# Kernel tuning notes

Measured on AMD Instinct MI355X. Metric: run time of the kernel, lower is better.

Reference implementation:

```python
import jax, jax.numpy as jnp
import numpy as np

B, W, C, N = 2, 2048, 512, 8
K = C // N                      # 64
HALF = K * (K + 1) // 2 - K     # strict upper-triangle count
EPS = 1e-5


def _layernorm(x, gamma, beta):
    mu = jnp.mean(x, axis=-1, keepdims=True)
    var = jnp.mean(jnp.square(x - mu), axis=-1, keepdims=True)
    return (x - mu) * jax.lax.rsqrt(var + EPS) * gamma + beta


def _build_metric(halves, diagonals):
    # symmetric per-head metric: strict upper triangle from `halves`,
    # mirrored, diagonal overwritten by `diagonals` (diag of m+m^T is 0).
    iu0, iu1 = np.triu_indices(K, k=1)
    m = jnp.zeros((N, K, K), dtype=halves.dtype).at[:, iu0, iu1].set(halves)
    m = m + jnp.swapaxes(m, -1, -2)
    d = np.arange(K)
    return m.at[:, d, d].set(diagonals)


def setup_inputs() -> dict:
    key = jax.random.key(0)
    ks = jax.random.split(key, 9)
    return {
        "x1": jax.random.normal(ks[0], (B, W, C), jnp.float32),
        "x2": jax.random.normal(ks[1], (B, W, C), jnp.float32),
        "gamma": jnp.ones((C,), jnp.float32),
        "beta": jnp.zeros((C,), jnp.float32),
        "proj_nck": jax.random.normal(ks[2], (N, C, K), jnp.float32) * (C ** -0.5),
        "halves": jax.random.normal(ks[3], (N, HALF), jnp.float32) * 0.05,
        "diagonals": jax.random.normal(ks[4], (N, K), jnp.float32) * 0.05,
        "W_mixer": jax.random.normal(ks[5], (C, C), jnp.float32) * 0.02,
        "b_mixer": jnp.zeros((C,), jnp.float32),
    }


def reference(x1, x2, gamma, beta, proj_nck, halves, diagonals, W_mixer, b_mixer):
    x1n = _layernorm(x1, gamma, beta)
    x2n = _layernorm(x2, gamma, beta)
    metric_nkk = _build_metric(halves, diagonals)

    # per-head projections (same projection used for both sequences)
    p1_bnwk = jnp.einsum("bwc,nck->bnwk", x1n, proj_nck)
    p2_bnwk = jnp.einsum("bwc,nck->bnwk", x2n, proj_nck)

    # bilinear metric scores  Q . M . K^T  -> [B, N, W, W]
    dots_bnww = jnp.einsum("bnwk,nkj,bnvj->bnwv", p1_bnwk, metric_nkk, p2_bnwk)

    # NOTE: the original computes a scaled/masked softmax of dots_bnww but
    # never uses it for the output; the value mix uses the RAW dot products.
    # We omit the dead softmax — output math is identical.

    nudged_bnwk = jnp.einsum("bnwv,bnvk->bnwk", dots_bnww, p1_bnwk)
    nudged_bwc = jnp.transpose(nudged_bnwk, (0, 2, 1, 3)).reshape(x1.shape[0], x1.shape[1], C)
    return nudged_bwc @ W_mixer.T + b_mixer
```

## Files before the change

kernel.cpp:

```cpp
#include <hip/hip_runtime.h>

typedef unsigned short u16;
typedef __attribute__((ext_vector_type(8))) short short8;
typedef __attribute__((ext_vector_type(4))) float f32x4;

#define HALFN 2016

__device__ __forceinline__ u16 f2b_rn(float x) {
    union { float f; unsigned u; } v; v.f = x;
    unsigned r = v.u + 0x7FFFu + ((v.u >> 16) & 1u);
    return (u16)(r >> 16);
}

__device__ __forceinline__ void gll16(const void* g, void* s) {
    __builtin_amdgcn_global_load_lds(
        (const __attribute__((address_space(1))) unsigned int*)g,
        (__attribute__((address_space(3))) unsigned int*)s, 16, 0, 0);
}

__global__ __launch_bounds__(256) void ln_prep(const float* __restrict__ x1,
                                               const float* __restrict__ x2,
                                               const float* __restrict__ gamma,
                                               const float* __restrict__ beta,
                                               const float* __restrict__ proj,
                                               u16* __restrict__ Xh,
                                               u16* __restrict__ Pwh,
                                               float* __restrict__ S) {
    const int bid = blockIdx.x, t = threadIdx.x;

    if (bid < 2048) {
        const int wv = t >> 6, lane = t & 63;
        const int row = bid * 4 + wv;
        const float* src = (row < 4096) ? (x1 + (size_t)row * 512)
                                        : (x2 + (size_t)(row - 4096) * 512);
        float4 v0 = *(const float4*)&src[lane * 4];
        float4 v1 = *(const float4*)&src[256 + lane * 4];
        float s  = v0.x + v0.y + v0.z + v0.w + v1.x + v1.y + v1.z + v1.w;
        float sq = v0.x * v0.x + v0.y * v0.y + v0.z * v0.z + v0.w * v0.w +
                   v1.x * v1.x + v1.y * v1.y + v1.z * v1.z + v1.w * v1.w;
        #pragma unroll
        for (int off = 32; off > 0; off >>= 1) {
            s  += __shfl_down(s, off);
            sq += __shfl_down(sq, off);
        }
        s  = __shfl(s, 0);
        sq = __shfl(sq, 0);
        float mu  = s * (1.0f / 512.0f);
        float var = sq * (1.0f / 512.0f) - mu * mu;
        float rs  = rsqrtf(var + 1e-5f);
        float4 g0 = *(const float4*)&gamma[lane * 4];
        float4 g1 = *(const float4*)&gamma[256 + lane * 4];
        float4 b0 = *(const float4*)&beta[lane * 4];
        float4 b1 = *(const float4*)&beta[256 + lane * 4];
        ushort4 h0, h1;
        h0.x = f2b_rn((v0.x - mu) * rs * g0.x + b0.x);
        h0.y = f2b_rn((v0.y - mu) * rs * g0.y + b0.y);
        h0.z = f2b_rn((v0.z - mu) * rs * g0.z + b0.z);
        h0.w = f2b_rn((v0.w - mu) * rs * g0.w + b0.w);
        h1.x = f2b_rn((v1.x - mu) * rs * g1.x + b1.x);
        h1.y = f2b_rn((v1.y - mu) * rs * g1.y + b1.y);
        h1.z = f2b_rn((v1.z - mu) * rs * g1.z + b1.z);
        h1.w = f2b_rn((v1.w - mu) * rs * g1.w + b1.w);
        *(ushort4*)&Xh[(size_t)row * 512 + lane * 4] = h0;
        *(ushort4*)&Xh[(size_t)row * 512 + 256 + lane * 4] = h1;
    } else if (bid < 2112) {
        __shared__ float tile[64][65];
        const int id = bid - 2048;
        const int n = id >> 3, c0 = (id & 7) * 64;
        #pragma unroll
        for (int i = 0; i < 4; i++) {
            int flat = i * 256 + t;
            int c = flat >> 4, k4 = (flat & 15) * 4;
            float4 v = *(const float4*)&proj[(size_t)n * 32768 + (size_t)(c0 + c) * 64 + k4];
            tile[c][k4 + 0] = v.x; tile[c][k4 + 1] = v.y;
            tile[c][k4 + 2] = v.z; tile[c][k4 + 3] = v.w;
        }
        __syncthreads();
        #pragma unroll
        for (int i = 0; i < 16; i++) {
            int flat = i * 256 + t;
            int k = flat >> 6, c = flat & 63;
            Pwh[(size_t)(n * 64 + k) * 512 + c0 + c] = f2b_rn(tile[c][k]);
        }
    } else {
        float4 z = {0.f, 0.f, 0.f, 0.f};
        #pragma unroll
        for (int i = 0; i < 64; i++)
            *(float4*)&S[(size_t)(i * 256 + t) * 4] = z;
    }
}

template<int TM, int TN>
__device__ __forceinline__ void gemm_core_bk64(const u16* __restrict__ A,
                                               const u16* __restrict__ B,
                                               int m0, int n0, int ld, u16* lds,
                                               f32x4 (&acc)[TM / 32][TN / 32]) {
    constexpr int MI = TM / 32, NI = TN / 32;
    constexpr int LA = TM * 64;
    const int t = threadIdx.x;
    const int lane = t & 63;
    const int w = t >> 6, wm = w & 1, wn = w >> 1;
    const int fr = lane & 15, q = lane >> 4;

    int aoff[2][MI], boff[2][NI];
    #pragma unroll
    for (int kc = 0; kc < 2; kc++) {
        #pragma unroll
        for (int i = 0; i < MI; i++) {
            int r = wm * (TM / 2) + i * 16 + fr;
            aoff[kc][i] = r * 64 + (((kc * 4 + q) ^ (r & 7)) * 8);
        }
        #pragma unroll
        for (int j = 0; j < NI; j++) {
            int r = wn * (TN / 2) + j * 16 + fr;
            boff[kc][j] = r * 64 + (((kc * 4 + q) ^ (r & 7)) * 8);
        }
    }

    for (int kt = 0; kt < 512; kt += 64) {
        #pragma unroll
        for (int p = 0; p < TM / 32; p++) {
            int o = p * 4096 + t * 16;
            int r = o >> 7;
            int c = ((o >> 4) & 7) ^ (r & 7);
            gll16(A + (size_t)(m0 + r) * ld + kt + c * 8, lds + (o >> 1));
        }
        #pragma unroll
        for (int p = 0; p < TN / 32; p++) {
            int o = p * 4096 + t * 16;
            int r = o >> 7;
            int c = ((o >> 4) & 7) ^ (r & 7);
            gll16(B + (size_t)(n0 + r) * ld + kt + c * 8, lds + LA + (o >> 1));
        }
        __syncthreads();
        #pragma unroll
        for (int kc = 0; kc < 2; kc++) {
            short8 af[MI], bf[NI];
            #pragma unroll
            for (int i = 0; i < MI; i++)
                af[i] = *(const short8*)(lds + aoff[kc][i]);
            #pragma unroll
            for (int j = 0; j < NI; j++)
                bf[j] = *(const short8*)(lds + LA + boff[kc][j]);
            #pragma unroll
            for (int i = 0; i < MI; i++)
                #pragma unroll
                for (int j = 0; j < NI; j++)
                    acc[i][j] = __builtin_amdgcn_mfma_f32_16x16x32_bf16(af[i], bf[j], acc[i][j], 0, 0, 0);
        }
        __syncthreads();
    }
}

__global__ __launch_bounds__(256) void gemm_proj_mfma(const u16* __restrict__ Xh,
                                                      const u16* __restrict__ Pwh,
                                                      u16* __restrict__ PPh,
                                                      u16* __restrict__ PPT1h,
                                                      u16* __restrict__ PPT2h) {
    __shared__ u16 lds[12288];
    f32x4 acc[4][2] = {};
    const int m0 = blockIdx.x * 128, n0 = blockIdx.y * 64;
    gemm_core_bk64<128, 64>(Xh, Pwh, m0, n0, 512, lds, acc);
    const int t = threadIdx.x, lane = t & 63, w = t >> 6, wm = w & 1, wn = w >> 1;
    const int fr = lane & 15, q = lane >> 4;
    const int src2 = (m0 >= 4096);
    const int b = (m0 & 4095) >> 11;
    const int v00 = m0 & 2047;
    #pragma unroll
    for (int i = 0; i < 4; i++) {
        int mloc = wm * 64 + i * 16 + q * 4;
        int v = v00 + mloc;
        #pragma unroll
        for (int j = 0; j < 2; j++) {
            int n = n0 + wn * 32 + j * 16 + fr;
            u16 hs[4];
            #pragma unroll
            for (int r = 0; r < 4; r++) hs[r] = f2b_rn(acc[i][j][r]);
            ushort4 hv; hv.x = hs[0]; hv.y = hs[1]; hv.z = hs[2]; hv.w = hs[3];
            if (!src2) {
                #pragma unroll
                for (int r = 0; r < 4; r++)
                    PPh[(size_t)(m0 + mloc + r) * 512 + n] = hs[r];
                *(ushort4*)&PPT1h[((size_t)(b * 512 + n)) * 2048 + v] = hv;
            } else {
                *(ushort4*)&PPT2h[((size_t)(b * 512 + n)) * 2048 + v] = hv;
            }
        }
    }
}

__global__ __launch_bounds__(256) void s_kernel(const u16* __restrict__ PPT2h,
                                                const u16* __restrict__ PPT1h,
                                                float* __restrict__ S) {
    __shared__ u16 lds[4096];
    const int bn = blockIdx.x, b = bn >> 3, n = bn & 7;
    const u16* A = PPT2h + ((size_t)(b * 512 + n * 64)) * 2048;
    const u16* B = PPT1h + ((size_t)(b * 512 + n * 64)) * 2048;
    const int t = threadIdx.x, lane = t & 63, w = t >> 6, wm = w & 1, wn = w >> 1;
    const int fr = lane & 15, q = lane >> 4;

    int aoff[2], boff[2];
    #pragma unroll
    for (int i = 0; i < 2; i++) {
        int r = wm * 32 + i * 16 + fr;
        aoff[i] = r * 32 + ((q ^ ((r >> 1) & 3)) * 8);
    }
    #pragma unroll
    for (int j = 0; j < 2; j++) {
        int r = wn * 32 + j * 16 + fr;
        boff[j] = r * 32 + ((q ^ ((r >> 1) & 3)) * 8);
    }
    const int o = t * 16;
    const int rr = o >> 6;
    const int kc = ((o >> 4) & 3) ^ ((rr >> 1) & 3);
    const int le = o >> 1;

    f32x4 acc[2][2] = {};
    const int k0 = blockIdx.y * 128;
    for (int kt = k0; kt < k0 + 128; kt += 32) {
        size_t g = (size_t)rr * 2048 + kt + kc * 8;
        gll16(A + g, lds + le);
        gll16(B + g, lds + 2048 + le);
        __syncthreads();
        short8 af[2], bf[2];
        #pragma unroll
        for (int i = 0; i < 2; i++) af[i] = *(const short8*)(lds + aoff[i]);
        #pragma unroll
        for (int j = 0; j < 2; j++) bf[j] = *(const short8*)(lds + 2048 + boff[j]);
        #pragma unroll
        for (int i = 0; i < 2; i++)
            #pragma unroll
            for (int j = 0; j < 2; j++)
                acc[i][j] = __builtin_amdgcn_mfma_f32_16x16x32_bf16(af[i], bf[j], acc[i][j], 0, 0, 0);
        __syncthreads();
    }
    float* Sb = S + (size_t)bn * 4096;
    #pragma unroll
    for (int i = 0; i < 2; i++) {
        int jrow = wm * 32 + i * 16 + q * 4;
        #pragma unroll
        for (int j = 0; j < 2; j++) {
            int kk = wn * 32 + j * 16 + fr;
            #pragma unroll
            for (int r = 0; r < 4; r++)
                atomicAdd(&Sb[(jrow + r) * 64 + kk], acc[i][j][r]);
        }
    }
}

__global__ __launch_bounds__(256) void tu_kernel(const float* __restrict__ S,
                                                 const float* __restrict__ halves,
                                                 const float* __restrict__ diagonals,
                                                 const float* __restrict__ Wm,
                                                 u16* __restrict__ UTh) {
    __shared__ float Ms[64][65];
    __shared__ float Gs[64][68];
    __shared__ float Ts[64][68];
    const int bid = blockIdx.x, t = threadIdx.x;
    const int bn = bid >> 3, b = bn >> 3, n = bn & 7, cy = bid & 7;

    for (int idx = t; idx < 4096; idx += 256) {
        int r = idx >> 6, c = idx & 63;
        float val;
        if (r == c) {
            val = diagonals[n * 64 + r];
        } else {
            int rr = (r < c) ? r : c;
            int cc = (r < c) ? c : r;
            int h = rr * 63 - (rr * (rr - 1)) / 2 + (cc - rr - 1);
            val = halves[n * HALFN + h];
        }
        Ms[r][c] = val;
    }
    for (int idx = t; idx < 4096; idx += 256)
        Gs[idx >> 6][idx & 63] = S[(size_t)bn * 4096 + idx];
    __syncthreads();

    {
        const int k = t & 63, lq = t >> 6;
        float a[16] = {};
        for (int j = 0; j < 64; j++) {
            float m = Ms[k][j];
            const float* gp = &Gs[j][lq * 16];
            #pragma unroll
            for (int u4 = 0; u4 < 4; u4++) {
                float4 g4 = *(const float4*)&gp[u4 * 4];
                a[u4 * 4 + 0] = fmaf(m, g4.x, a[u4 * 4 + 0]);
                a[u4 * 4 + 1] = fmaf(m, g4.y, a[u4 * 4 + 1]);
                a[u4 * 4 + 2] = fmaf(m, g4.z, a[u4 * 4 + 2]);
                a[u4 * 4 + 3] = fmaf(m, g4.w, a[u4 * 4 + 3]);
            }
        }
        int pos = (lq ^ (k & 3)) * 16;
        #pragma unroll
        for (int u4 = 0; u4 < 4; u4++) {
            float4 v4 = {a[u4 * 4 + 0], a[u4 * 4 + 1], a[u4 * 4 + 2], a[u4 * 4 + 3]};
            *(float4*)&Ts[k][pos + u4 * 4] = v4;
        }
    }
    __syncthreads();

    const int k2 = t & 63, cgp = t >> 6;
    const int c0 = cy * 64 + cgp * 16;
    float uacc[16] = {};
    #pragma unroll
    for (int kkc = 0; kkc < 4; kkc++) {
        const float* tp = &Ts[k2][(kkc ^ (k2 & 3)) * 16];
        float ts[16];
        #pragma unroll
        for (int u = 0; u < 4; u++) {
            float4 t4 = *(const float4*)&tp[u * 4];
            ts[u * 4 + 0] = t4.x; ts[u * 4 + 1] = t4.y;
            ts[u * 4 + 2] = t4.z; ts[u * 4 + 3] = t4.w;
        }
        #pragma unroll
        for (int i = 0; i < 16; i++) {
            const float* wrow = &Wm[(size_t)(c0 + i) * 512 + n * 64 + kkc * 16];
            #pragma unroll
            for (int u = 0; u < 4; u++) {
                float4 w4 = *(const float4*)&wrow[u * 4];
                uacc[i] = fmaf(ts[u * 4 + 0], w4.x, uacc[i]);
                uacc[i] = fmaf(ts[u * 4 + 1], w4.y, uacc[i]);
                uacc[i] = fmaf(ts[u * 4 + 2], w4.z, uacc[i]);
                uacc[i] = fmaf(ts[u * 4 + 3], w4.w, uacc[i]);
            }
        }
    }
    #pragma unroll
    for (int i = 0; i < 16; i++)
        UTh[(size_t)b * 262144 + (size_t)(c0 + i) * 512 + n * 64 + k2] = f2b_rn(uacc[i]);
}

__global__ __launch_bounds__(256) void gemm_out_mfma(const u16* __restrict__ PPh,
                                                     const u16* __restrict__ UTh,
                                                     const float* __restrict__ bias,
                                                     float* __restrict__ out) {
    __shared__ u16 lds[8192];
    const int b = blockIdx.z;
    const u16* A = PPh + (size_t)b * 2048 * 512;
    const u16* B = UTh + (size_t)b * 512 * 512;
    f32x4 acc[2][2] = {};
    const int m0 = blockIdx.x * 64, n0 = blockIdx.y * 64;
    gemm_core_bk64<64, 64>(A, B, m0, n0, 512, lds, acc);
    const int t = threadIdx.x, lane = t & 63, w = t >> 6, wm = w & 1, wn = w >> 1;
    const int fr = lane & 15, q = lane >> 4;
    #pragma unroll
    for (int i = 0; i < 2; i++) {
        int m = m0 + wm * 32 + i * 16 + q * 4;
        #pragma unroll
        for (int j = 0; j < 2; j++) {
            int n = n0 + wn * 32 + j * 16 + fr;
            float bv = bias[n];
            #pragma unroll
            for (int r = 0; r < 4; r++)
                out[(size_t)(b * 2048 + m + r) * 512 + n] = acc[i][j][r] + bv;
        }
    }
}

extern "C" void kernel_launch(void* const* d_in, const int* in_sizes, int n_in,
                              void* d_out, int out_size, void* d_ws, size_t ws_size,
                              hipStream_t stream) {
    (void)in_sizes; (void)n_in; (void)out_size; (void)ws_size;
    const float* x1        = (const float*)d_in[0];
    const float* x2        = (const float*)d_in[1];
    const float* gamma     = (const float*)d_in[2];
    const float* beta      = (const float*)d_in[3];
    const float* proj      = (const float*)d_in[4];
    const float* halves    = (const float*)d_in[5];
    const float* diagonals = (const float*)d_in[6];
    const float* Wm        = (const float*)d_in[7];
    const float* bmix      = (const float*)d_in[8];
    float* out = (float*)d_out;

    u16* us    = (u16*)d_ws;
    u16* Xh    = us;
    u16* Pwh   = Xh + 4194304;
    u16* PPh   = Pwh + 262144;
    u16* PPT1h = PPh + 2097152;
    u16* PPT2h = PPT1h + 2097152;
    u16* UTh   = PPT2h + 2097152;
    float* S   = (float*)(UTh + 524288);

    ln_prep<<<dim3(2113), 256, 0, stream>>>(x1, x2, gamma, beta, proj, Xh, Pwh, S);
    gemm_proj_mfma<<<dim3(64, 8), 256, 0, stream>>>(Xh, Pwh, PPh, PPT1h, PPT2h);
    s_kernel<<<dim3(16, 16), 256, 0, stream>>>(PPT2h, PPT1h, S);
    tu_kernel<<<dim3(128), 256, 0, stream>>>(S, halves, diagonals, Wm, UTh);
    gemm_out_mfma<<<dim3(32, 8, 2), 256, 0, stream>>>(PPh, UTh, bmix, out);
}
```

Before: 123.8 us.

## Fuse projection GEMM with per-head Gram accumulation, drop transposed buffers

The projection GEMM and the S (P2^T·P1 per head) kernel become one kernel. Each block computes matching 64-row tiles of both projected sequences for one head, stages them in LDS, and multiplies them to get a partial Gram matrix that is atomically added into S. This removes the transposed PPT1/PPT2 global writes, their re-reads, and one kernel launch. In exchange there are more float atomics into S (one set per 64-row block instead of per 128-wide k split), and each block's tile shape changes.

```diff
diff --git a/kernel.cpp b/kernel.cpp
--- a/kernel.cpp
+++ b/kernel.cpp
@@ -152,89 +152,117 @@
     }
 }
 
-__global__ __launch_bounds__(256) void gemm_proj_mfma(const u16* __restrict__ Xh,
-                                                      const u16* __restrict__ Pwh,
-                                                      u16* __restrict__ PPh,
-                                                      u16* __restrict__ PPT1h,
-                                                      u16* __restrict__ PPT2h) {
+__global__ __launch_bounds__(256) void proj_g_mfma(const u16* __restrict__ Xh,
+                                                   const u16* __restrict__ Pwh,
+                                                   u16* __restrict__ PPh,
+                                                   float* __restrict__ S) {
     __shared__ u16 lds[12288];
-    f32x4 acc[4][2] = {};
-    const int m0 = blockIdx.x * 128, n0 = blockIdx.y * 64;
-    gemm_core_bk64<128, 64>(Xh, Pwh, m0, n0, 512, lds, acc);
+    const int bx = blockIdx.x;
+    const int n  = blockIdx.y;
+    const int b = bx >> 5, v0 = (bx & 31) * 64;
+    const u16* A1 = Xh + (size_t)(b * 2048 + v0) * 512;
+    const u16* A2 = A1 + (size_t)4096 * 512;
+    const u16* Bp = Pwh + (size_t)(n * 64) * 512;
+
     const int t = threadIdx.x, lane = t & 63, w = t >> 6, wm = w & 1, wn = w >> 1;
     const int fr = lane & 15, q = lane >> 4;
-    const int src2 = (m0 >= 4096);
-    const int b = (m0 & 4095) >> 11;
-    const int v00 = m0 & 2047;
-    #pragma unroll
-    for (int i = 0; i < 4; i++) {
-        int mloc = wm * 64 + i * 16 + q * 4;
-        int v = v00 + mloc;
+
+    int aoff[2][2], boff[2][2];
+    #pragma unroll
+    for (int kc = 0; kc < 2; kc++) {
+        #pragma unroll
+        for (int i = 0; i < 2; i++) {
+            int r = wm * 32 + i * 16 + fr;
+            aoff[kc][i] = r * 64 + (((kc * 4 + q) ^ (r & 7)) * 8);
+        }
         #pragma unroll
         for (int j = 0; j < 2; j++) {
-            int n = n0 + wn * 32 + j * 16 + fr;
-            u16 hs[4];
-            #pragma unroll
-            for (int r = 0; r < 4; r++) hs[r] = f2b_rn(acc[i][j][r]);
-            ushort4 hv; hv.x = hs[0]; hv.y = hs[1]; hv.z = hs[2]; hv.w = hs[3];
-            if (!src2) {
+            int r = wn * 32 + j * 16 + fr;
+            boff[kc][j] = r * 64 + (((kc * 4 + q) ^ (r & 7)) * 8);
+        }
+    }
+
+    f32x4 acc1[2][2] = {}, acc2[2][2] = {};
+    const int o0 = t * 16;
+    for (int kt = 0; kt < 512; kt += 64) {
+        #pragma unroll
+        for (int p = 0; p < 2; p++) {
+            int o = p * 4096 + o0;
+            int r = o >> 7;
+            int c = ((o >> 4) & 7) ^ (r & 7);
+            size_t g = (size_t)r * 512 + kt + c * 8;
+            gll16(A1 + g, lds + (o >> 1));
+            gll16(A2 + g, lds + 4096 + (o >> 1));
+            gll16(Bp + g, lds + 8192 + (o >> 1));
+        }
+        __syncthreads();
+        #pragma unroll
+        for (int kc = 0; kc < 2; kc++) {
+            short8 a1f[2], a2f[2], bf[2];
+            #pragma unroll
+            for (int i = 0; i < 2; i++) {
+                a1f[i] = *(const short8*)(lds + aoff[kc][i]);
+                a2f[i] = *(const short8*)(lds + 4096 + aoff[kc][i]);
+            }
+            #pragma unroll
+            for (int j = 0; j < 2; j++)
+                bf[j] = *(const short8*)(lds + 8192 + boff[kc][j]);
+            #pragma unroll
+            for (int i = 0; i < 2; i++)
                 #pragma unroll
-                for (int r = 0; r < 4; r++)
-                    PPh[(size_t)(m0 + mloc + r) * 512 + n] = hs[r];
-                *(ushort4*)&PPT1h[((size_t)(b * 512 + n)) * 2048 + v] = hv;
-            } else {
-                *(ushort4*)&PPT2h[((size_t)(b * 512 + n)) * 2048 + v] = hv;
+                for (int j = 0; j < 2; j++) {
+                    acc1[i][j] = __builtin_amdgcn_mfma_f32_16x16x32_bf16(a1f[i], bf[j], acc1[i][j], 0, 0, 0);
+                    acc2[i][j] = __builtin_amdgcn_mfma_f32_16x16x32_bf16(a2f[i], bf[j], acc2[i][j], 0, 0, 0);
+                }
+        }
+        __syncthreads();
+    }
+
+    #pragma unroll
+    for (int i = 0; i < 2; i++) {
+        const int mloc = wm * 32 + i * 16 + q * 4;
+        #pragma unroll
+        for (int j = 0; j < 2; j++) {
+            const int c = wn * 32 + j * 16 + fr;
+            u16 h1[4], h2[4];
+            #pragma unroll
+            for (int r = 0; r < 4; r++) {
+                h1[r] = f2b_rn(acc1[i][j][r]);
+                h2[r] = f2b_rn(acc2[i][j][r]);
             }
-        }
-    }
-}
-
-__global__ __launch_bounds__(256) void s_kernel(const u16* __restrict__ PPT2h,
-                                                const u16* __restrict__ PPT1h,
-                                                float* __restrict__ S) {
-    __shared__ u16 lds[4096];
-    const int bn = blockIdx.x, b = bn >> 3, n = bn & 7;
-    const u16* A = PPT2h + ((size_t)(b * 512 + n * 64)) * 2048;
-    const u16* B = PPT1h + ((size_t)(b * 512 + n * 64)) * 2048;
-    const int t = threadIdx.x, lane = t & 63, w = t >> 6, wm = w & 1, wn = w >> 1;
-    const int fr = lane & 15, q = lane >> 4;
-
-    int aoff[2], boff[2];
-    #pragma unroll
-    for (int i = 0; i < 2; i++) {
-        int r = wm * 32 + i * 16 + fr;
-        aoff[i] = r * 32 + ((q ^ ((r >> 1) & 3)) * 8);
-    }
-    #pragma unroll
-    for (int j = 0; j < 2; j++) {
-        int r = wn * 32 + j * 16 + fr;
-        boff[j] = r * 32 + ((q ^ ((r >> 1) & 3)) * 8);
-    }
-    const int o = t * 16;
-    const int rr = o >> 6;
-    const int kc = ((o >> 4) & 3) ^ ((rr >> 1) & 3);
-    const int le = o >> 1;
-
-    f32x4 acc[2][2] = {};
-    const int k0 = blockIdx.y * 128;
-    for (int kt = k0; kt < k0 + 128; kt += 32) {
-        size_t g = (size_t)rr * 2048 + kt + kc * 8;
-        gll16(A + g, lds + le);
-        gll16(B + g, lds + 2048 + le);
-        __syncthreads();
-        short8 af[2], bf[2];
-        #pragma unroll
-        for (int i = 0; i < 2; i++) af[i] = *(const short8*)(lds + aoff[i]);
-        #pragma unroll
-        for (int j = 0; j < 2; j++) bf[j] = *(const short8*)(lds + 2048 + boff[j]);
+            #pragma unroll
+            for (int r = 0; r < 4; r++)
+                PPh[(size_t)(b * 2048 + v0 + mloc + r) * 512 + n * 64 + c] = h1[r];
+            const int sw = c * 64 + (((mloc >> 3) ^ (c & 7)) * 8) + (mloc & 7);
+            ushort4 u1; u1.x = h1[0]; u1.y = h1[1]; u1.z = h1[2]; u1.w = h1[3];
+            ushort4 u2; u2.x = h2[0]; u2.y = h2[1]; u2.z = h2[2]; u2.w = h2[3];
+            *(ushort4*)&lds[sw] = u1;
+            *(ushort4*)&lds[4096 + sw] = u2;
+        }
+    }
+    __syncthreads();
+
+    f32x4 accg[2][2] = {};
+    #pragma unroll
+    for (int ks = 0; ks < 2; ks++) {
+        short8 ag[2], bg[2];
+        #pragma unroll
+        for (int i = 0; i < 2; i++) {
+            int jr = wm * 32 + i * 16 + fr;
+            ag[i] = *(const short8*)&lds[4096 + jr * 64 + (((ks * 4 + q) ^ (jr & 7)) * 8)];
+        }
+        #pragma unroll
+        for (int j = 0; j < 2; j++) {
+            int kr = wn * 32 + j * 16 + fr;
+            bg[j] = *(const short8*)&lds[kr * 64 + (((ks * 4 + q) ^ (kr & 7)) * 8)];
+        }
         #pragma unroll
         for (int i = 0; i < 2; i++)
             #pragma unroll
             for (int j = 0; j < 2; j++)
-                acc[i][j] = __builtin_amdgcn_mfma_f32_16x16x32_bf16(af[i], bf[j], acc[i][j], 0, 0, 0);
-        __syncthreads();
-    }
-    float* Sb = S + (size_t)bn * 4096;
+                accg[i][j] = __builtin_amdgcn_mfma_f32_16x16x32_bf16(ag[i], bg[j], accg[i][j], 0, 0, 0);
+    }
+    float* Sb = S + (size_t)(b * 8 + n) * 4096;
     #pragma unroll
     for (int i = 0; i < 2; i++) {
         int jrow = wm * 32 + i * 16 + q * 4;
@@ -243,7 +271,7 @@
             int kk = wn * 32 + j * 16 + fr;
             #pragma unroll
             for (int r = 0; r < 4; r++)
-                atomicAdd(&Sb[(jrow + r) * 64 + kk], acc[i][j][r]);
+                atomicAdd(&Sb[(jrow + r) * 64 + kk], accg[i][j][r]);
         }
     }
 }
@@ -377,14 +405,11 @@
     u16* Xh    = us;
     u16* Pwh   = Xh + 4194304;
     u16* PPh   = Pwh + 262144;
-    u16* PPT1h = PPh + 2097152;
-    u16* PPT2h = PPT1h + 2097152;
-    u16* UTh   = PPT2h + 2097152;
+    u16* UTh   = PPh + 2097152;
     float* S   = (float*)(UTh + 524288);
 
     ln_prep<<<dim3(2113), 256, 0, stream>>>(x1, x2, gamma, beta, proj, Xh, Pwh, S);
-    gemm_proj_mfma<<<dim3(64, 8), 256, 0, stream>>>(Xh, Pwh, PPh, PPT1h, PPT2h);
-    s_kernel<<<dim3(16, 16), 256, 0, stream>>>(PPT2h, PPT1h, S);
+    proj_g_mfma<<<dim3(64, 8), 256, 0, stream>>>(Xh, Pwh, PPh, S);
     tu_kernel<<<dim3(128), 256, 0, stream>>>(S, halves, diagonals, Wm, UTh);
     gemm_out_mfma<<<dim3(32, 8, 2), 256, 0, stream>>>(PPh, UTh, bmix, out);
 }
```

After: 121.1 us. -2.1%, faster.
